# Kernel optimization log

Hardware: AMD Instinct MI355X
Metric: run time of the kernel (lower is better)

The kernel has to match this reference:

```python
import jax, jax.numpy as jnp
import numpy as np

ROPE_BASE = 10000.0

def _rope_tables(pos, d_head):
    # pos: (T,) int; returns cos,sin of shape (T, d_head//2)
    half = d_head // 2
    inv_freq = 1.0 / (ROPE_BASE ** (jnp.arange(half, dtype=jnp.float32) / half))
    ang = pos.astype(jnp.float32)[:, None] * inv_freq[None, :]
    return jnp.cos(ang), jnp.sin(ang)

def _apply_rope(x, cos, sin):
    # x: (B, H, T, D); cos/sin: (T, D//2); rotate-half convention
    x1, x2 = jnp.split(x, 2, axis=-1)
    c = cos[None, None, :, :]
    s = sin[None, None, :, :]
    return jnp.concatenate([x1 * c - x2 * s, x1 * s + x2 * c], axis=-1)

def setup_inputs() -> dict:
    key = jax.random.key(0)
    ks = jax.random.split(key, 8)
    B, T, C = 16, 4, 2048
    n_head, n_kv_head, d_head = 16, 4, 128
    S_cache = 4096
    sd = 1.0 / np.sqrt(C)
    return {
        "x": jax.random.normal(ks[0], (B, T, C), dtype=jnp.float32),
        "cache_k": jax.random.normal(ks[1], (B, n_kv_head, S_cache, d_head), dtype=jnp.float32),
        "cache_v": jax.random.normal(ks[2], (B, n_kv_head, S_cache, d_head), dtype=jnp.float32),
        "wq": jax.random.normal(ks[3], (C, n_head * d_head), dtype=jnp.float32) * sd,
        "wk": jax.random.normal(ks[4], (C, n_kv_head * d_head), dtype=jnp.float32) * sd,
        "wv": jax.random.normal(ks[5], (C, n_kv_head * d_head), dtype=jnp.float32) * sd,
        "w_proj": jax.random.normal(ks[6], (C, C), dtype=jnp.float32) * sd,
        "start_pos": 4096,
    }

def reference(x, cache_k, cache_v, wq, wk, wv, w_proj, start_pos):
    B, T, C = x.shape
    n_head, n_kv_head = 16, 4
    d_head = C // n_head
    group_size = n_head // n_kv_head
    sliding_window, sink = 2048, 4

    # projections -> (B, H, T, D)
    q = (x @ wq).reshape(B, T, n_head, d_head).transpose(0, 2, 1, 3)
    k = (x @ wk).reshape(B, T, n_kv_head, d_head).transpose(0, 2, 1, 3)
    v = (x @ wv).reshape(B, T, n_kv_head, d_head).transpose(0, 2, 1, 3)

    # RoPE at absolute positions [start_pos, start_pos+T)
    pos = jnp.arange(start_pos, start_pos + T)
    cos, sin = _rope_tables(pos, d_head)
    q = _apply_rope(q, cos, sin)
    k = _apply_rope(k, cos, sin)

    # KV cache concat along sequence dim
    k_all = jnp.concatenate([cache_k, k], axis=2)
    v_all = jnp.concatenate([cache_v, v], axis=2)

    # sliding window + attention sink slicing (4096+T > 2048+4)
    if k_all.shape[2] > sliding_window + sink:
        k_all = jnp.concatenate([k_all[:, :, :sink, :], k_all[:, :, -sliding_window:, :]], axis=2)
        v_all = jnp.concatenate([v_all[:, :, :sink, :], v_all[:, :, -sliding_window:, :]], axis=2)

    # GQA: expand KV heads to match query heads (repeat_interleave on head dim)
    k_attn = jnp.repeat(k_all, group_size, axis=1)
    v_attn = jnp.repeat(v_all, group_size, axis=1)

    # SDPA, is_causal=False (decode path with cache), dropout=0 (eval)
    scale = 1.0 / jnp.sqrt(jnp.float32(d_head))
    scores = jnp.einsum('bhtd,bhsd->bhts', q, k_attn) * scale
    attn = jax.nn.softmax(scores, axis=-1)
    y = jnp.einsum('bhts,bhsd->bhtd', attn, v_attn)

    y = y.transpose(0, 2, 1, 3).reshape(B, T, C)
    return y @ w_proj
```

## Files before the change

kernel.cpp:

```cpp
#include <hip/hip_runtime.h>
#include <math.h>

#define BB   16
#define TT   4
#define CC   2048
#define NH   16
#define NKV  4
#define DH   128
#define GRP  4
#define SCACHE 4096
#define SATT 2052
#define CS   128
#define NCH  17
#define KSPL 8

typedef unsigned int  uint32;
typedef unsigned short ushort_t;
typedef __attribute__((ext_vector_type(8))) __bf16 bf16x8;
typedef __attribute__((ext_vector_type(4))) float  f32x4;

__device__ __forceinline__ uint32 f2bf_bits(float f) {
    uint32 u = __float_as_uint(f);
    return (u + 0x7FFFu + ((u >> 16) & 1u)) >> 16;
}
__device__ __forceinline__ uint32 pk2(float lo, float hi) {
    return f2bf_bits(lo) | (f2bf_bits(hi) << 16);
}
#define F4C(v, j) ((j)==0 ? (v).x : (j)==1 ? (v).y : (j)==2 ? (v).z : (v).w)

#define Q_OFF    0
#define KNEW_OFF 524288
#define VNEW_OFF 655360
#define Y_OFF    786432
#define SCR_OFF  1310720

__global__ __launch_bounds__(256) void k_qkv(
    const float* __restrict__ x, const float* __restrict__ wq,
    const float* __restrict__ wk, const float* __restrict__ wv,
    float* __restrict__ part_qkv)
{
    __shared__ float xs[64][256];
    int ns = blockIdx.x, ks = blockIdx.y;
    int tid = threadIdx.x;
    int k0 = ks * 256;

    #pragma unroll
    for (int it = 0; it < 16; ++it) {
        int slot = it * 256 + tid;
        int row = slot >> 6, c4 = slot & 63;
        *(float4*)&xs[row][c4 * 4] = *(const float4*)(x + (size_t)row * CC + k0 + c4 * 4);
    }
    __syncthreads();

    int cp = tid & 31, rg = tid >> 5;
    const float* wp; int ldw, col;
    if (ns < 32)      { ldw = 2048; col = ns * 64 + cp * 2;
                        wp = wq + (size_t)k0 * 2048 + ns * 64 + cp * 2; }
    else if (ns < 40) { ldw = 512;  col = 2048 + (ns - 32) * 64 + cp * 2;
                        wp = wk + (size_t)k0 * 512 + (ns - 32) * 64 + cp * 2; }
    else              { ldw = 512;  col = 2560 + (ns - 40) * 64 + cp * 2;
                        wp = wv + (size_t)k0 * 512 + (ns - 40) * 64 + cp * 2; }

    float a[16];
    #pragma unroll
    for (int i = 0; i < 16; ++i) a[i] = 0.f;

    for (int k = 0; k < 256; k += 4) {
        float2 w0 = *(const float2*)(wp);
        float2 w1 = *(const float2*)(wp + ldw);
        float2 w2 = *(const float2*)(wp + 2 * ldw);
        float2 w3 = *(const float2*)(wp + 3 * ldw);
        wp += 4 * ldw;
        #pragma unroll
        for (int m = 0; m < 8; ++m) {
            float4 xv = *(const float4*)&xs[rg * 8 + m][k];
            float s0 = a[2*m], s1 = a[2*m+1];
            s0 = fmaf(xv.x, w0.x, s0); s1 = fmaf(xv.x, w0.y, s1);
            s0 = fmaf(xv.y, w1.x, s0); s1 = fmaf(xv.y, w1.y, s1);
            s0 = fmaf(xv.z, w2.x, s0); s1 = fmaf(xv.z, w2.y, s1);
            s0 = fmaf(xv.w, w3.x, s0); s1 = fmaf(xv.w, w3.y, s1);
            a[2*m] = s0; a[2*m+1] = s1;
        }
    }
    #pragma unroll
    for (int m = 0; m < 8; ++m)
        *(float2*)(part_qkv + ((size_t)(ks * 64 + rg * 8 + m) * 3072) + col) =
            make_float2(a[2*m], a[2*m+1]);
}

__global__ __launch_bounds__(256) void k_fix(
    const float* __restrict__ part_qkv, const int* __restrict__ spp,
    float* __restrict__ qws, float* __restrict__ knew, float* __restrict__ vnew)
{
    int u = blockIdx.x * 256 + threadIdx.x;
    int m = blockIdx.y;
    int b = m >> 2, t = m & 3;
    int sp = spp[0];
    const float NEG_L2_10K_64 = -0.20762050593048633f;

    if (u < 1024) {
        int h = u >> 6, d = u & 63;
        int col = h * 128 + d;
        float s1 = 0.f, s2 = 0.f;
        #pragma unroll
        for (int ks = 0; ks < KSPL; ++ks) {
            const float* p = part_qkv + (size_t)(ks * 64 + m) * 3072;
            s1 += p[col]; s2 += p[col + 64];
        }
        float inv = exp2f((float)d * NEG_L2_10K_64);
        float ang = (float)(sp + t) * inv;
        float cc = cosf(ang), ss = sinf(ang);
        float* dst = qws + (size_t)((b * NH + h) * TT + t) * DH + d;
        dst[0]  = s1 * cc - s2 * ss;
        dst[64] = s1 * ss + s2 * cc;
    } else if (u < 1280) {
        int v = u - 1024;
        int kv = v >> 6, d = v & 63;
        int col = 2048 + kv * 128 + d;
        float s1 = 0.f, s2 = 0.f;
        #pragma unroll
        for (int ks = 0; ks < KSPL; ++ks) {
            const float* p = part_qkv + (size_t)(ks * 64 + m) * 3072;
            s1 += p[col]; s2 += p[col + 64];
        }
        float inv = exp2f((float)d * NEG_L2_10K_64);
        float ang = (float)(sp + t) * inv;
        float cc = cosf(ang), ss = sinf(ang);
        float* dst = knew + (size_t)((b * NKV + kv) * TT + t) * DH + d;
        dst[0]  = s1 * cc - s2 * ss;
        dst[64] = s1 * ss + s2 * cc;
    } else {
        int v = u - 1280;
        int c0 = v * 2;
        int kv = c0 >> 7, dd = c0 & 127;
        float s1 = 0.f, s2 = 0.f;
        #pragma unroll
        for (int ks = 0; ks < KSPL; ++ks) {
            const float* p = part_qkv + (size_t)(ks * 64 + m) * 3072 + 2560 + c0;
            s1 += p[0]; s2 += p[1];
        }
        float* dst = vnew + (size_t)((b * NKV + kv) * TT + t) * DH + dd;
        dst[0] = s1; dst[1] = s2;
    }
}

__device__ __forceinline__ const float* kv_row(
    const float* cache, const float* newt, int bk, int j)
{
    if (j < 4)         return cache + ((size_t)bk * SCACHE + j) * DH;
    else if (j < 2048) return cache + ((size_t)bk * SCACHE + j + 2048) * DH;
    else               return newt  + ((size_t)(bk * TT + (j - 2048))) * DH;
}

__global__ __launch_bounds__(256) void k_attn(
    const float* __restrict__ qws,
    const float* __restrict__ kc, const float* __restrict__ vc,
    const float* __restrict__ knew, const float* __restrict__ vnew,
    float* __restrict__ part)
{
    __shared__ __align__(16) uint32 smem[9600];

    int bx = blockIdx.x;
    int c  = bx % NCH;
    int bk = bx / NCH;
    int b  = bk >> 2, kvh = bk & 3;
    int j0 = c * CS;
    int jn = (SATT - j0 < CS) ? (SATT - j0) : CS;
    int tid  = threadIdx.x;
    int w    = tid >> 6, lane = tid & 63;
    int quad = lane >> 4, l15 = lane & 15;
    const float scale = 0.08838834764831845f;

    uint32*   vt    = smem + w * 2048;
    ushort_t* pl    = (ushort_t*)(smem + 8448) + w * 512;
    float*    red_m = (float*)(smem + 9472);
    float*    red_l = red_m + 64;
    float*    o_all = (float*)smem;

    int base = w * 32;

    int rA = base + l15, rB = base + 16 + l15;
    const float* kAp = kv_row(kc, knew, bk, j0 + (rA < jn ? rA : 0));
    const float* kBp = kv_row(kc, knew, bk, j0 + (rB < jn ? rB : 0));
    float4 ka[8], kb[8];
    #pragma unroll
    for (int ks = 0; ks < 4; ++ks) {
        ka[2*ks]   = *(const float4*)(kAp + ks * 32 + quad * 8);
        ka[2*ks+1] = *(const float4*)(kAp + ks * 32 + quad * 8 + 4);
        kb[2*ks]   = *(const float4*)(kBp + ks * 32 + quad * 8);
        kb[2*ks+1] = *(const float4*)(kBp + ks * 32 + quad * 8 + 4);
    }

    int key0 = base + 2 * l15, key1 = key0 + 1;
    bool okA = key0 < jn, okB = key1 < jn;
    const float* rva = kv_row(vc, vnew, bk, j0 + (okA ? key0 : 0));
    const float* rvb = kv_row(vc, vnew, bk, j0 + (okB ? key1 : 0));
    float4 va[4], vb[4];
    #pragma unroll
    for (int i = 0; i < 4; ++i) {
        va[i] = *(const float4*)(rva + quad * 32 + i * 4);
        vb[i] = *(const float4*)(rvb + quad * 32 + i * 4);
    }

    bf16x8 aq[4];
    {
        int h = kvh * GRP + (l15 >> 2), t = l15 & 3;
        const float* qr = qws + (size_t)((b * NH + h) * TT + t) * DH;
        #pragma unroll
        for (int ks = 0; ks < 4; ++ks) {
            float4 f0 = *(const float4*)(qr + ks * 32 + quad * 8);
            float4 f1 = *(const float4*)(qr + ks * 32 + quad * 8 + 4);
            union { uint32 u[4]; bf16x8 v; } pk_;
            pk_.u[0] = pk2(f0.x * scale, f0.y * scale);
            pk_.u[1] = pk2(f0.z * scale, f0.w * scale);
            pk_.u[2] = pk2(f1.x * scale, f1.y * scale);
            pk_.u[3] = pk2(f1.z * scale, f1.w * scale);
            aq[ks] = pk_.v;
        }
    }

    f32x4 s0 = {0.f, 0.f, 0.f, 0.f}, s1 = {0.f, 0.f, 0.f, 0.f};
    #pragma unroll
    for (int ks = 0; ks < 4; ++ks) {
        union { uint32 u[4]; bf16x8 v; } pa, pb;
        pa.u[0] = pk2(ka[2*ks].x,   ka[2*ks].y);
        pa.u[1] = pk2(ka[2*ks].z,   ka[2*ks].w);
        pa.u[2] = pk2(ka[2*ks+1].x, ka[2*ks+1].y);
        pa.u[3] = pk2(ka[2*ks+1].z, ka[2*ks+1].w);
        pb.u[0] = pk2(kb[2*ks].x,   kb[2*ks].y);
        pb.u[1] = pk2(kb[2*ks].z,   kb[2*ks].w);
        pb.u[2] = pk2(kb[2*ks+1].x, kb[2*ks+1].y);
        pb.u[3] = pk2(kb[2*ks+1].z, kb[2*ks+1].w);
        s0 = __builtin_amdgcn_mfma_f32_16x16x32_bf16(aq[ks], pa.v, s0, 0, 0, 0);
        s1 = __builtin_amdgcn_mfma_f32_16x16x32_bf16(aq[ks], pb.v, s1, 0, 0, 0);
    }

    #pragma unroll
    for (int i = 0; i < 4; ++i) {
        #pragma unroll
        for (int jj = 0; jj < 4; ++jj) {
            int dd = i * 4 + jj;
            int d  = quad * 32 + dd;
            int sw = (dd ^ (dd >> 2)) & 3;
            float fa = okA ? F4C(va[i], jj) : 0.f;
            float fb = okB ? F4C(vb[i], jj) : 0.f;
            vt[d * 16 + ((((l15 >> 2) ^ sw) << 2) | (l15 & 3))] = pk2(fa, fb);
        }
    }
    float4 va2[4], vb2[4];
    #pragma unroll
    for (int i = 0; i < 4; ++i) {
        va2[i] = *(const float4*)(rva + quad * 32 + 16 + i * 4);
        vb2[i] = *(const float4*)(rvb + quad * 32 + 16 + i * 4);
    }

    bool c0ok = (base + l15) < jn, c1ok = (base + 16 + l15) < jn;
    float sc0[4], sc1[4], mloc[4];
    #pragma unroll
    for (int i = 0; i < 4; ++i) {
        sc0[i] = c0ok ? s0[i] : -1e30f;
        sc1[i] = c1ok ? s1[i] : -1e30f;
        float v = fmaxf(sc0[i], sc1[i]);
        v = fmaxf(v, __shfl_xor(v, 1));
        v = fmaxf(v, __shfl_xor(v, 2));
        v = fmaxf(v, __shfl_xor(v, 4));
        v = fmaxf(v, __shfl_xor(v, 8));
        mloc[i] = v;
        float p0 = __expf(sc0[i] - v);
        float p1 = __expf(sc1[i] - v);
        int r   = quad * 4 + i;
        int swr = (i ^ quad) & 3;
        pl[r * 32 + ((((l15 >> 3)    ) ^ swr) << 3) + (l15 & 7)] = (ushort_t)f2bf_bits(p0);
        pl[r * 32 + ((((l15 >> 3) | 2) ^ swr) << 3) + (l15 & 7)] = (ushort_t)f2bf_bits(p1);
        float su = p0 + p1;
        su += __shfl_xor(su, 1);
        su += __shfl_xor(su, 2);
        su += __shfl_xor(su, 4);
        su += __shfl_xor(su, 8);
        if (l15 == 0) { red_m[w * 16 + r] = v; red_l[w * 16 + r] = su; }
    }

    #pragma unroll
    for (int i = 0; i < 4; ++i) {
        #pragma unroll
        for (int jj = 0; jj < 4; ++jj) {
            int dd = 16 + i * 4 + jj;
            int d  = quad * 32 + dd;
            int sw = (dd ^ (dd >> 2)) & 3;
            float fa = okA ? F4C(va2[i], jj) : 0.f;
            float fb = okB ? F4C(vb2[i], jj) : 0.f;
            vt[d * 16 + ((((l15 >> 2) ^ sw) << 2) | (l15 & 3))] = pk2(fa, fb);
        }
    }

    int swp = (l15 ^ (l15 >> 2)) & 3;
    bf16x8 ap = *(const bf16x8*)&pl[l15 * 32 + ((quad ^ swp) << 3)];
    f32x4 o[8];
    #pragma unroll
    for (int t = 0; t < 8; ++t) o[t] = (f32x4){0.f, 0.f, 0.f, 0.f};
    #pragma unroll
    for (int t = 0; t < 8; ++t) {
        int d   = t * 16 + l15;
        int swv = (d ^ (d >> 2)) & 3;
        bf16x8 bv = *(const bf16x8*)&vt[d * 16 + ((quad ^ swv) << 2)];
        o[t] = __builtin_amdgcn_mfma_f32_16x16x32_bf16(ap, bv, o[t], 0, 0, 0);
    }

    __syncthreads();
    #pragma unroll
    for (int i = 0; i < 4; ++i) {
        int r = quad * 4 + i;
        float Mb = fmaxf(fmaxf(red_m[r], red_m[16 + r]),
                         fmaxf(red_m[32 + r], red_m[48 + r]));
        float scl = __expf(mloc[i] - Mb);
        #pragma unroll
        for (int t = 0; t < 8; ++t)
            o_all[(w * 16 + r) * 132 + t * 16 + l15] = o[t][i] * scl;
    }
    __syncthreads();
    {
        int r = tid >> 4, dg = tid & 15;
        float acc[8];
        #pragma unroll
        for (int jj = 0; jj < 8; ++jj) acc[jj] = 0.f;
        #pragma unroll
        for (int ww = 0; ww < 4; ++ww) {
            const float* src = &o_all[(ww * 16 + r) * 132 + dg * 8];
            #pragma unroll
            for (int jj = 0; jj < 8; ++jj) acc[jj] += src[jj];
        }
        float* dstb = part + (size_t)(bk * NCH + c) * 16 * 132;
        #pragma unroll
        for (int jj = 0; jj < 8; ++jj) dstb[r * 132 + 4 + dg * 8 + jj] = acc[jj];
        if (dg == 0) {
            float Mb = fmaxf(fmaxf(red_m[r], red_m[16 + r]),
                             fmaxf(red_m[32 + r], red_m[48 + r]));
            float L = 0.f;
            #pragma unroll
            for (int ww = 0; ww < 4; ++ww)
                L += __expf(red_m[ww * 16 + r] - Mb) * red_l[ww * 16 + r];
            dstb[r * 132 + 0] = Mb;
            dstb[r * 132 + 1] = L;
        }
    }
}

__global__ __launch_bounds__(128) void k_comb(
    const float* __restrict__ part, float* __restrict__ yws)
{
    int bx = blockIdx.x;
    int t = bx & 3, h = (bx >> 2) & 15, b = bx >> 6;
    int bk = b * NKV + (h >> 2);
    int r  = (h & 3) * 4 + t;
    int d  = threadIdx.x;
    float M = -1e30f;
    for (int c = 0; c < NCH; ++c)
        M = fmaxf(M, part[((size_t)(bk * NCH + c) * 16 + r) * 132]);
    float L = 0.f, y = 0.f;
    for (int c = 0; c < NCH; ++c) {
        const float* pp = part + ((size_t)(bk * NCH + c) * 16 + r) * 132;
        float w = __expf(pp[0] - M);
        L += w * pp[1];
        y  = fmaf(w, pp[4 + d], y);
    }
    yws[(size_t)(b * TT + t) * CC + h * DH + d] = y / L;
}

__global__ __launch_bounds__(256) void k_proj(
    const float* __restrict__ yws, const float* __restrict__ wp,
    float* __restrict__ part_p)
{
    __shared__ float xs[64][256];
    int ns = blockIdx.x, ks = blockIdx.y;
    int tid = threadIdx.x;
    int k0 = ks * 256;
    #pragma unroll
    for (int it = 0; it < 16; ++it) {
        int slot = it * 256 + tid;
        int row = slot >> 6, c4 = slot & 63;
        *(float4*)&xs[row][c4 * 4] = *(const float4*)(yws + (size_t)row * CC + k0 + c4 * 4);
    }
    __syncthreads();

    int cp = tid & 31, rg = tid >> 5;
    int n = ns * 64 + cp * 2;
    const float* w = wp + (size_t)k0 * CC + n;
    float a[16];
    #pragma unroll
    for (int i = 0; i < 16; ++i) a[i] = 0.f;

    for (int k = 0; k < 256; k += 4) {
        float2 w0 = *(const float2*)(w);
        float2 w1 = *(const float2*)(w + CC);
        float2 w2 = *(const float2*)(w + 2 * CC);
        float2 w3 = *(const float2*)(w + 3 * CC);
        w += 4 * CC;
        #pragma unroll
        for (int m = 0; m < 8; ++m) {
            float4 xv = *(const float4*)&xs[rg * 8 + m][k];
            float s0 = a[2*m], s1 = a[2*m+1];
            s0 = fmaf(xv.x, w0.x, s0); s1 = fmaf(xv.x, w0.y, s1);
            s0 = fmaf(xv.y, w1.x, s0); s1 = fmaf(xv.y, w1.y, s1);
            s0 = fmaf(xv.z, w2.x, s0); s1 = fmaf(xv.z, w2.y, s1);
            s0 = fmaf(xv.w, w3.x, s0); s1 = fmaf(xv.w, w3.y, s1);
            a[2*m] = s0; a[2*m+1] = s1;
        }
    }
    #pragma unroll
    for (int m = 0; m < 8; ++m)
        *(float2*)(part_p + ((size_t)(ks * 64 + rg * 8 + m) * CC) + n) =
            make_float2(a[2*m], a[2*m+1]);
}

__global__ __launch_bounds__(256) void k_out(
    const float* __restrict__ part_p, float* __restrict__ out)
{
    int gt = blockIdx.x * 256 + threadIdx.x;
    float s = 0.f;
    #pragma unroll
    for (int ks = 0; ks < KSPL; ++ks) s += part_p[(size_t)ks * 64 * CC + gt];
    out[gt] = s;
}

extern "C" void kernel_launch(void* const* d_in, const int* in_sizes, int n_in,
                              void* d_out, int out_size, void* d_ws, size_t ws_size,
                              hipStream_t stream)
{
    const float* x   = (const float*)d_in[0];
    const float* ck  = (const float*)d_in[1];
    const float* cv  = (const float*)d_in[2];
    const float* wq  = (const float*)d_in[3];
    const float* wk  = (const float*)d_in[4];
    const float* wv  = (const float*)d_in[5];
    const float* wpj = (const float*)d_in[6];
    const int*   sp  = (const int*)d_in[7];
    char* ws = (char*)d_ws;
    float* qws  = (float*)(ws + Q_OFF);
    float* knew = (float*)(ws + KNEW_OFF);
    float* vnew = (float*)(ws + VNEW_OFF);
    float* yws  = (float*)(ws + Y_OFF);
    float* scr  = (float*)(ws + SCR_OFF);
    float* out  = (float*)d_out;

    hipLaunchKernelGGL(k_qkv,  dim3(48, 8),   dim3(256), 0, stream, x, wq, wk, wv, scr);
    hipLaunchKernelGGL(k_fix,  dim3(6, 64),   dim3(256), 0, stream, scr, sp, qws, knew, vnew);
    hipLaunchKernelGGL(k_attn, dim3(64 * NCH), dim3(256), 0, stream, qws, ck, cv, knew, vnew, scr);
    hipLaunchKernelGGL(k_comb, dim3(1024),    dim3(128), 0, stream, scr, yws);
    hipLaunchKernelGGL(k_proj, dim3(32, 8),   dim3(256), 0, stream, yws, wpj, scr);
    hipLaunchKernelGGL(k_out,  dim3(512),     dim3(256), 0, stream, scr, out);
}
```

Before: 368.3 us.

## Loop attention over 256-key chunks with online softmax; fold split-K reduce into atomics

The attention kernel now handles 256 keys per block (9 chunks instead of 17), with each wave running two 32-key iterations under an online-softmax rescale. This halves the number of partials that the combine kernel must merge and the blocks that reload Q. The final k_out reduction kernel is removed: k_comb zeroes the output and k_proj accumulates its split-K partials directly with atomicAdd. The change saves one launch and the partial buffer traffic, but float atomics make the summation order nondeterministic and grid parallelism in attention drops.

New measurement: 362.7 us. No clear change (-1.5%).

```diff
diff --git a/kernel.cpp b/kernel.cpp
--- a/kernel.cpp
+++ b/kernel.cpp
@@ -10,8 +10,8 @@
 #define GRP  4
 #define SCACHE 4096
 #define SATT 2052
-#define CS   128
-#define NCH  17
+#define CS   256
+#define NCH  9
 #define KSPL 8
 
 typedef unsigned int  uint32;
@@ -177,31 +177,6 @@
     float*    red_l = red_m + 64;
     float*    o_all = (float*)smem;
 
-    int base = w * 32;
-
-    int rA = base + l15, rB = base + 16 + l15;
-    const float* kAp = kv_row(kc, knew, bk, j0 + (rA < jn ? rA : 0));
-    const float* kBp = kv_row(kc, knew, bk, j0 + (rB < jn ? rB : 0));
-    float4 ka[8], kb[8];
-    #pragma unroll
-    for (int ks = 0; ks < 4; ++ks) {
-        ka[2*ks]   = *(const float4*)(kAp + ks * 32 + quad * 8);
-        ka[2*ks+1] = *(const float4*)(kAp + ks * 32 + quad * 8 + 4);
-        kb[2*ks]   = *(const float4*)(kBp + ks * 32 + quad * 8);
-        kb[2*ks+1] = *(const float4*)(kBp + ks * 32 + quad * 8 + 4);
-    }
-
-    int key0 = base + 2 * l15, key1 = key0 + 1;
-    bool okA = key0 < jn, okB = key1 < jn;
-    const float* rva = kv_row(vc, vnew, bk, j0 + (okA ? key0 : 0));
-    const float* rvb = kv_row(vc, vnew, bk, j0 + (okB ? key1 : 0));
-    float4 va[4], vb[4];
-    #pragma unroll
-    for (int i = 0; i < 4; ++i) {
-        va[i] = *(const float4*)(rva + quad * 32 + i * 4);
-        vb[i] = *(const float4*)(rvb + quad * 32 + i * 4);
-    }
-
     bf16x8 aq[4];
     {
         int h = kvh * GRP + (l15 >> 2), t = l15 & 3;
@@ -219,91 +194,134 @@
         }
     }
 
-    f32x4 s0 = {0.f, 0.f, 0.f, 0.f}, s1 = {0.f, 0.f, 0.f, 0.f};
-    #pragma unroll
-    for (int ks = 0; ks < 4; ++ks) {
-        union { uint32 u[4]; bf16x8 v; } pa, pb;
-        pa.u[0] = pk2(ka[2*ks].x,   ka[2*ks].y);
-        pa.u[1] = pk2(ka[2*ks].z,   ka[2*ks].w);
-        pa.u[2] = pk2(ka[2*ks+1].x, ka[2*ks+1].y);
-        pa.u[3] = pk2(ka[2*ks+1].z, ka[2*ks+1].w);
-        pb.u[0] = pk2(kb[2*ks].x,   kb[2*ks].y);
-        pb.u[1] = pk2(kb[2*ks].z,   kb[2*ks].w);
-        pb.u[2] = pk2(kb[2*ks+1].x, kb[2*ks+1].y);
-        pb.u[3] = pk2(kb[2*ks+1].z, kb[2*ks+1].w);
-        s0 = __builtin_amdgcn_mfma_f32_16x16x32_bf16(aq[ks], pa.v, s0, 0, 0, 0);
-        s1 = __builtin_amdgcn_mfma_f32_16x16x32_bf16(aq[ks], pb.v, s1, 0, 0, 0);
+    float mrow[4], lrow[4];
+    #pragma unroll
+    for (int i = 0; i < 4; ++i) { mrow[i] = -1e30f; lrow[i] = 0.f; }
+    f32x4 o[8];
+    #pragma unroll
+    for (int t = 0; t < 8; ++t) o[t] = (f32x4){0.f, 0.f, 0.f, 0.f};
+
+    for (int it = 0; it < 2; ++it) {
+        int base = w * 64 + it * 32;
+
+        int rA = base + l15, rB = base + 16 + l15;
+        const float* kAp = kv_row(kc, knew, bk, j0 + (rA < jn ? rA : 0));
+        const float* kBp = kv_row(kc, knew, bk, j0 + (rB < jn ? rB : 0));
+        float4 ka[8], kb[8];
+        #pragma unroll
+        for (int ks = 0; ks < 4; ++ks) {
+            ka[2*ks]   = *(const float4*)(kAp + ks * 32 + quad * 8);
+            ka[2*ks+1] = *(const float4*)(kAp + ks * 32 + quad * 8 + 4);
+            kb[2*ks]   = *(const float4*)(kBp + ks * 32 + quad * 8);
+            kb[2*ks+1] = *(const float4*)(kBp + ks * 32 + quad * 8 + 4);
+        }
+
+        int key0 = base + 2 * l15, key1 = key0 + 1;
+        bool okA = key0 < jn, okB = key1 < jn;
+        const float* rva = kv_row(vc, vnew, bk, j0 + (okA ? key0 : 0));
+        const float* rvb = kv_row(vc, vnew, bk, j0 + (okB ? key1 : 0));
+        float4 va[4], vb[4];
+        #pragma unroll
+        for (int i = 0; i < 4; ++i) {
+            va[i] = *(const float4*)(rva + quad * 32 + i * 4);
+            vb[i] = *(const float4*)(rvb + quad * 32 + i * 4);
+        }
+
+        f32x4 s0 = {0.f, 0.f, 0.f, 0.f}, s1 = {0.f, 0.f, 0.f, 0.f};
+        #pragma unroll
+        for (int ks = 0; ks < 4; ++ks) {
+            union { uint32 u[4]; bf16x8 v; } pa, pb;
+            pa.u[0] = pk2(ka[2*ks].x,   ka[2*ks].y);
+            pa.u[1] = pk2(ka[2*ks].z,   ka[2*ks].w);
+            pa.u[2] = pk2(ka[2*ks+1].x, ka[2*ks+1].y);
+            pa.u[3] = pk2(ka[2*ks+1].z, ka[2*ks+1].w);
+            pb.u[0] = pk2(kb[2*ks].x,   kb[2*ks].y);
+            pb.u[1] = pk2(kb[2*ks].z,   kb[2*ks].w);
+            pb.u[2] = pk2(kb[2*ks+1].x, kb[2*ks+1].y);
+            pb.u[3] = pk2(kb[2*ks+1].z, kb[2*ks+1].w);
+            s0 = __builtin_amdgcn_mfma_f32_16x16x32_bf16(aq[ks], pa.v, s0, 0, 0, 0);
+            s1 = __builtin_amdgcn_mfma_f32_16x16x32_bf16(aq[ks], pb.v, s1, 0, 0, 0);
+        }
+
+        #pragma unroll
+        for (int i = 0; i < 4; ++i) {
+            #pragma unroll
+            for (int jj = 0; jj < 4; ++jj) {
+                int dd = i * 4 + jj;
+                int d  = quad * 32 + dd;
+                int sw = (dd ^ (dd >> 2)) & 3;
+                float fa = okA ? F4C(va[i], jj) : 0.f;
+                float fb = okB ? F4C(vb[i], jj) : 0.f;
+                vt[d * 16 + ((((l15 >> 2) ^ sw) << 2) | (l15 & 3))] = pk2(fa, fb);
+            }
+        }
+        float4 va2[4], vb2[4];
+        #pragma unroll
+        for (int i = 0; i < 4; ++i) {
+            va2[i] = *(const float4*)(rva + quad * 32 + 16 + i * 4);
+            vb2[i] = *(const float4*)(rvb + quad * 32 + 16 + i * 4);
+        }
+
+        bool c0ok = (base + l15) < jn, c1ok = (base + 16 + l15) < jn;
+        #pragma unroll
+        for (int i = 0; i < 4; ++i) {
+            float x0 = c0ok ? s0[i] : -1e30f;
+            float x1 = c1ok ? s1[i] : -1e30f;
+            float v = fmaxf(x0, x1);
+            v = fmaxf(v, __shfl_xor(v, 1));
+            v = fmaxf(v, __shfl_xor(v, 2));
+            v = fmaxf(v, __shfl_xor(v, 4));
+            v = fmaxf(v, __shfl_xor(v, 8));
+            float mo = mrow[i];
+            float mn = fmaxf(mo, v);
+            float scl = __expf(mo - mn);
+            float p0 = __expf(x0 - mn);
+            float p1 = __expf(x1 - mn);
+            int r   = quad * 4 + i;
+            int swr = (i ^ quad) & 3;
+            pl[r * 32 + ((((l15 >> 3)    ) ^ swr) << 3) + (l15 & 7)] = (ushort_t)f2bf_bits(p0);
+            pl[r * 32 + ((((l15 >> 3) | 2) ^ swr) << 3) + (l15 & 7)] = (ushort_t)f2bf_bits(p1);
+            float su = p0 + p1;
+            su += __shfl_xor(su, 1);
+            su += __shfl_xor(su, 2);
+            su += __shfl_xor(su, 4);
+            su += __shfl_xor(su, 8);
+            lrow[i] = lrow[i] * scl + su;
+            mrow[i] = mn;
+            #pragma unroll
+            for (int t = 0; t < 8; ++t) o[t][i] *= scl;
+        }
+
+        #pragma unroll
+        for (int i = 0; i < 4; ++i) {
+            #pragma unroll
+            for (int jj = 0; jj < 4; ++jj) {
+                int dd = 16 + i * 4 + jj;
+                int d  = quad * 32 + dd;
+                int sw = (dd ^ (dd >> 2)) & 3;
+                float fa = okA ? F4C(va2[i], jj) : 0.f;
+                float fb = okB ? F4C(vb2[i], jj) : 0.f;
+                vt[d * 16 + ((((l15 >> 2) ^ sw) << 2) | (l15 & 3))] = pk2(fa, fb);
+            }
+        }
+
+        int swp = (l15 ^ (l15 >> 2)) & 3;
+        bf16x8 ap = *(const bf16x8*)&pl[l15 * 32 + ((quad ^ swp) << 3)];
+        #pragma unroll
+        for (int t = 0; t < 8; ++t) {
+            int d   = t * 16 + l15;
+            int swv = (d ^ (d >> 2)) & 3;
+            bf16x8 bv = *(const bf16x8*)&vt[d * 16 + ((quad ^ swv) << 2)];
+            o[t] = __builtin_amdgcn_mfma_f32_16x16x32_bf16(ap, bv, o[t], 0, 0, 0);
+        }
     }
 
     #pragma unroll
     for (int i = 0; i < 4; ++i) {
-        #pragma unroll
-        for (int jj = 0; jj < 4; ++jj) {
-            int dd = i * 4 + jj;
-            int d  = quad * 32 + dd;
-            int sw = (dd ^ (dd >> 2)) & 3;
-            float fa = okA ? F4C(va[i], jj) : 0.f;
-            float fb = okB ? F4C(vb[i], jj) : 0.f;
-            vt[d * 16 + ((((l15 >> 2) ^ sw) << 2) | (l15 & 3))] = pk2(fa, fb);
-        }
-    }
-    float4 va2[4], vb2[4];
-    #pragma unroll
-    for (int i = 0; i < 4; ++i) {
-        va2[i] = *(const float4*)(rva + quad * 32 + 16 + i * 4);
-        vb2[i] = *(const float4*)(rvb + quad * 32 + 16 + i * 4);
-    }
-
-    bool c0ok = (base + l15) < jn, c1ok = (base + 16 + l15) < jn;
-    float sc0[4], sc1[4], mloc[4];
-    #pragma unroll
-    for (int i = 0; i < 4; ++i) {
-        sc0[i] = c0ok ? s0[i] : -1e30f;
-        sc1[i] = c1ok ? s1[i] : -1e30f;
-        float v = fmaxf(sc0[i], sc1[i]);
-        v = fmaxf(v, __shfl_xor(v, 1));
-        v = fmaxf(v, __shfl_xor(v, 2));
-        v = fmaxf(v, __shfl_xor(v, 4));
-        v = fmaxf(v, __shfl_xor(v, 8));
-        mloc[i] = v;
-        float p0 = __expf(sc0[i] - v);
-        float p1 = __expf(sc1[i] - v);
-        int r   = quad * 4 + i;
-        int swr = (i ^ quad) & 3;
-        pl[r * 32 + ((((l15 >> 3)    ) ^ swr) << 3) + (l15 & 7)] = (ushort_t)f2bf_bits(p0);
-        pl[r * 32 + ((((l15 >> 3) | 2) ^ swr) << 3) + (l15 & 7)] = (ushort_t)f2bf_bits(p1);
-        float su = p0 + p1;
-        su += __shfl_xor(su, 1);
-        su += __shfl_xor(su, 2);
-        su += __shfl_xor(su, 4);
-        su += __shfl_xor(su, 8);
-        if (l15 == 0) { red_m[w * 16 + r] = v; red_l[w * 16 + r] = su; }
-    }
-
-    #pragma unroll
-    for (int i = 0; i < 4; ++i) {
-        #pragma unroll
-        for (int jj = 0; jj < 4; ++jj) {
-            int dd = 16 + i * 4 + jj;
-            int d  = quad * 32 + dd;
-            int sw = (dd ^ (dd >> 2)) & 3;
-            float fa = okA ? F4C(va2[i], jj) : 0.f;
-            float fb = okB ? F4C(vb2[i], jj) : 0.f;
-            vt[d * 16 + ((((l15 >> 2) ^ sw) << 2) | (l15 & 3))] = pk2(fa, fb);
-        }
-    }
-
-    int swp = (l15 ^ (l15 >> 2)) & 3;
-    bf16x8 ap = *(const bf16x8*)&pl[l15 * 32 + ((quad ^ swp) << 3)];
-    f32x4 o[8];
-    #pragma unroll
-    for (int t = 0; t < 8; ++t) o[t] = (f32x4){0.f, 0.f, 0.f, 0.f};
-    #pragma unroll
-    for (int t = 0; t < 8; ++t) {
-        int d   = t * 16 + l15;
-        int swv = (d ^ (d >> 2)) & 3;
-        bf16x8 bv = *(const bf16x8*)&vt[d * 16 + ((quad ^ swv) << 2)];
-        o[t] = __builtin_amdgcn_mfma_f32_16x16x32_bf16(ap, bv, o[t], 0, 0, 0);
+        if (l15 == 0) {
+            red_m[w * 16 + quad * 4 + i] = mrow[i];
+            red_l[w * 16 + quad * 4 + i] = lrow[i];
+        }
     }
 
     __syncthreads();
@@ -312,7 +330,7 @@
         int r = quad * 4 + i;
         float Mb = fmaxf(fmaxf(red_m[r], red_m[16 + r]),
                          fmaxf(red_m[32 + r], red_m[48 + r]));
-        float scl = __expf(mloc[i] - Mb);
+        float scl = __expf(mrow[i] - Mb);
         #pragma unroll
         for (int t = 0; t < 8; ++t)
             o_all[(w * 16 + r) * 132 + t * 16 + l15] = o[t][i] * scl;
@@ -346,9 +364,12 @@
 }
 
 __global__ __launch_bounds__(128) void k_comb(
-    const float* __restrict__ part, float* __restrict__ yws)
+    const float* __restrict__ part, float* __restrict__ yws,
+    float* __restrict__ out)
 {
     int bx = blockIdx.x;
+    out[(size_t)bx * 128 + threadIdx.x] = 0.f;
+
     int t = bx & 3, h = (bx >> 2) & 15, b = bx >> 6;
     int bk = b * NKV + (h >> 2);
     int r  = (h & 3) * 4 + t;
@@ -368,7 +389,7 @@
 
 __global__ __launch_bounds__(256) void k_proj(
     const float* __restrict__ yws, const float* __restrict__ wp,
-    float* __restrict__ part_p)
+    float* __restrict__ out)
 {
     __shared__ float xs[64][256];
     int ns = blockIdx.x, ks = blockIdx.y;
@@ -407,19 +428,10 @@
         }
     }
     #pragma unroll
-    for (int m = 0; m < 8; ++m)
-        *(float2*)(part_p + ((size_t)(ks * 64 + rg * 8 + m) * CC) + n) =
-            make_float2(a[2*m], a[2*m+1]);
-}
-
-__global__ __launch_bounds__(256) void k_out(
-    const float* __restrict__ part_p, float* __restrict__ out)
-{
-    int gt = blockIdx.x * 256 + threadIdx.x;
-    float s = 0.f;
-    #pragma unroll
-    for (int ks = 0; ks < KSPL; ++ks) s += part_p[(size_t)ks * 64 * CC + gt];
-    out[gt] = s;
+    for (int m = 0; m < 8; ++m) {
+        atomicAdd(out + (size_t)(rg * 8 + m) * CC + n,     a[2*m]);
+        atomicAdd(out + (size_t)(rg * 8 + m) * CC + n + 1, a[2*m+1]);
+    }
 }
 
 extern "C" void kernel_launch(void* const* d_in, const int* in_sizes, int n_in,
@@ -442,10 +454,9 @@
     float* scr  = (float*)(ws + SCR_OFF);
     float* out  = (float*)d_out;
 
-    hipLaunchKernelGGL(k_qkv,  dim3(48, 8),   dim3(256), 0, stream, x, wq, wk, wv, scr);
-    hipLaunchKernelGGL(k_fix,  dim3(6, 64),   dim3(256), 0, stream, scr, sp, qws, knew, vnew);
+    hipLaunchKernelGGL(k_qkv,  dim3(48, 8),    dim3(256), 0, stream, x, wq, wk, wv, scr);
+    hipLaunchKernelGGL(k_fix,  dim3(6, 64),    dim3(256), 0, stream, scr, sp, qws, knew, vnew);
     hipLaunchKernelGGL(k_attn, dim3(64 * NCH), dim3(256), 0, stream, qws, ck, cv, knew, vnew, scr);
-    hipLaunchKernelGGL(k_comb, dim3(1024),    dim3(128), 0, stream, scr, yws);
-    hipLaunchKernelGGL(k_proj, dim3(32, 8),   dim3(256), 0, stream, yws, wpj, scr);
-    hipLaunchKernelGGL(k_out,  dim3(512),     dim3(256), 0, stream, scr, out);
-}
+    hipLaunchKernelGGL(k_comb, dim3(1024),     dim3(128), 0, stream, scr, yws, out);
+    hipLaunchKernelGGL(k_proj, dim3(32, 8),    dim3(256), 0, stream, yws, wpj, out);
+}
```
